# Performance work log

Hardware: AMD Instinct MI355X
Metric: run time of the kernel (lower is better)

## Reference

```python
import jax, jax.numpy as jnp
import numpy as np

B, C, D, H, EXP = 4, 1024, 1024, 16, 4
EPS = 1e-6


def ffn_layernorm(x, w, b):
    # normalize over channel axis (dim 1); w,b have shape (1, C)
    u = jnp.mean(x, axis=1, keepdims=True)
    s = jnp.mean((x - u) ** 2, axis=1, keepdims=True)
    xn = (x - u) / jnp.sqrt(s + EPS)
    return w[:, :, None] * xn + b[:, :, None]


def softmax_one(x):
    # exp(x - max) / (1 + sum exp(x - max)), exactly as the torch SoftmaxOne
    m = jnp.max(x, axis=-1, keepdims=True)
    e = jnp.exp(x - m)
    return e / (1.0 + jnp.sum(e, axis=-1, keepdims=True))


def setup_inputs() -> dict:
    key = jax.random.key(0)
    ks = jax.random.split(key, 20)
    n = lambda k, shape, s=0.02: jax.random.normal(k, shape, dtype=jnp.float32) * s
    inp = {
        "x1": jax.random.normal(ks[0], (B, C, D), dtype=jnp.float32),
        "lnq_w": jnp.ones((1, C), jnp.float32) + n(ks[1], (1, C)),
        "lnq_b": n(ks[2], (1, C)),
        "lnk_w": jnp.ones((1, C), jnp.float32) + n(ks[3], (1, C)),
        "lnk_b": n(ks[4], (1, C)),
        "lnv_w": jnp.ones((1, C), jnp.float32) + n(ks[5], (1, C)),
        "lnv_b": n(ks[6], (1, C)),
        "wq": n(ks[7], (D, D)),
        "bq": n(ks[8], (D,)),
        "wk": n(ks[9], (D, D)),
        "bk": n(ks[10], (D,)),
        "wv": n(ks[11], (D, D)),
        "bv": n(ks[12], (D,)),
        "ffnln_w": jnp.ones((1, C), jnp.float32) + n(ks[13], (1, C)),
        "ffnln_b": n(ks[14], (1, C)),
        "conv1_w": n(ks[15], (C * EXP, C)),
        "conv1_b": n(ks[16], (C * EXP,)),
        "conv2_w": n(ks[17], (C, C * EXP)),
        "conv2_b": n(ks[18], (C,)),
    }
    return inp


def reference(x1, lnq_w, lnq_b, lnk_w, lnk_b, lnv_w, lnv_b,
              wq, bq, wk, bk, wv, bv,
              ffnln_w, ffnln_b, conv1_w, conv1_b, conv2_w, conv2_b):
    b, c, d = x1.shape
    dh = d // H
    q = ffn_layernorm(x1, lnq_w, lnq_b)
    k = ffn_layernorm(x1, lnk_w, lnk_b)
    v = ffn_layernorm(x1, lnv_w, lnv_b)
    # nn.Linear: y = x @ W.T + b, then the torch code's direct reshape
    # (b, c, d) -> (b, H, c, dh) (NOT a transpose-split)
    q = (q @ wq.T + bq).reshape(b, H, c, dh)
    k = (k @ wk.T + bk).reshape(b, H, c, dh)
    v = (v @ wv.T + bv).reshape(b, H, c, dh)
    scale = 1.0 / np.sqrt(dh).astype(np.float32)
    attn = jnp.einsum("bhqe,bhke->bhqk", q * scale, k)
    attn_weights = softmax_one(attn)
    o = jnp.einsum("bhqk,bhke->bhqe", attn_weights, v)
    o = o.transpose(0, 2, 1, 3).reshape(b, c, d)
    x = x1 + o
    # FFN: channel LayerNorm -> 1x1 conv (channel mix) -> GELU -> 1x1 conv
    xl = ffn_layernorm(x, ffnln_w, ffnln_b)
    h1 = jnp.einsum("oc,bcl->bol", conv1_w, xl) + conv1_b[None, :, None]
    h1 = jax.nn.gelu(h1, approximate=False)
    h2 = jnp.einsum("oc,bcl->bol", conv2_w, h1) + conv2_b[None, :, None]
    return (x + h2, attn_weights)
```

## Files before the change

kernel.cpp:

```cpp
#include <hip/hip_runtime.h>
#include <hip/hip_bf16.h>
#include <math.h>


typedef __bf16 bf16;
typedef __bf16 bf16x4 __attribute__((ext_vector_type(4)));
typedef __bf16 bf16x8 __attribute__((ext_vector_type(8)));
typedef float floatx4 __attribute__((ext_vector_type(4)));

#define MFMA16(a, b, c) __builtin_amdgcn_mfma_f32_16x16x32_bf16(a, b, c, 0, 0, 0)

__device__ __forceinline__ void gload16(const void* g, void* l) {
    __builtin_amdgcn_global_load_lds((__attribute__((address_space(1))) void*)g,
                                     (__attribute__((address_space(3))) void*)l,
                                     16, 0, 0);
}

__global__ __launch_bounds__(256)
void cast_all(const float* __restrict__ s0, bf16* __restrict__ d0_,
              const float* __restrict__ s1, bf16* __restrict__ d1_,
              const float* __restrict__ s2, bf16* __restrict__ d2_,
              const float* __restrict__ s3, bf16* __restrict__ d3_,
              const float* __restrict__ s4, bf16* __restrict__ d4_,
              float* __restrict__ rsumout)
{
    __shared__ float S[64][4];
    const int blk = blockIdx.x;
    const int tid = threadIdx.x;
    if (blk >= 11264) {
        const int j = blk - 11264;
        const int seg = j >> 4;
        const int obase = (j & 15) << 6;
        const float* W = seg == 0 ? s0 : (seg == 1 ? s1 : s2);
        float* outr = rsumout + (seg << 10);
        const int lane = tid & 63, wv_ = tid >> 6;
        for (int oi = 0; oi < 64; ++oi) {
            const float4 w4 = *(const float4*)(W + ((long)(obase + oi) << 10) + (tid << 2));
            float p = w4.x + w4.y + w4.z + w4.w;
#pragma unroll
            for (int off = 1; off < 64; off <<= 1) p += __shfl_xor(p, off, 64);
            if (lane == 0) S[oi][wv_] = p;
        }
        __syncthreads();
        if (tid < 64)
            outr[obase + tid] = S[tid][0] + S[tid][1] + S[tid][2] + S[tid][3];
        return;
    }
    const float* s; bf16* d; int base;
    if (blk < 1024)      { s = s0; d = d0_; base = blk; }
    else if (blk < 2048) { s = s1; d = d1_; base = blk - 1024; }
    else if (blk < 3072) { s = s2; d = d2_; base = blk - 2048; }
    else if (blk < 7168) { s = s3; d = d3_; base = blk - 3072; }
    else                 { s = s4; d = d4_; base = blk - 7168; }
    long i = ((long)base << 10) + (tid << 2);
    float4 v = *(const float4*)(s + i);
    bf16x4 o;
    o[0] = (bf16)v.x; o[1] = (bf16)v.y; o[2] = (bf16)v.z; o[3] = (bf16)v.w;
    *(bf16x4*)(d + i) = o;
}

__global__ __launch_bounds__(256)
void stats_part(const float* __restrict__ xin, float* __restrict__ ps,
                float* __restrict__ pq)
{
    __shared__ float S1[4][64];
    __shared__ float S2[4][64];
    const int b = blockIdx.z, chunk = blockIdx.y;
    const int d0 = blockIdx.x << 6;
    const int tid = threadIdx.x;
    const int dl = tid & 63, cg = tid >> 6;
    const float* xp = xin + ((long)b << 20) + d0 + dl;
    const int cbase = (chunk << 8) + (cg << 6);
    float s = 0.f, sq = 0.f;
    for (int c = 0; c < 64; ++c) {
        float v = xp[(long)(cbase + c) << 10];
        s += v; sq += v * v;
    }
    S1[cg][dl] = s; S2[cg][dl] = sq;
    __syncthreads();
    if (tid < 64) {
        float ts = S1[0][tid] + S1[1][tid] + S1[2][tid] + S1[3][tid];
        float tq = S2[0][tid] + S2[1][tid] + S2[2][tid] + S2[3][tid];
        int idx = ((b * 4 + chunk) << 10) + d0 + tid;
        ps[idx] = ts; pq[idx] = tq;
    }
}

__global__ __launch_bounds__(256)
void ln_x1_kernel(const float* __restrict__ x1, const float* __restrict__ ps,
                  const float* __restrict__ pq, bf16* __restrict__ xn)
{
    const int bc = blockIdx.x;
    const int b = bc >> 10;
    const int d = threadIdx.x << 2;
    const long i = ((long)bc << 10) + d;
    const float* pb = ps + (b << 12) + d;
    const float* qb = pq + (b << 12) + d;
    float s0 = 0.f, s1 = 0.f, s2 = 0.f, s3 = 0.f;
    float q0 = 0.f, q1 = 0.f, q2 = 0.f, q3 = 0.f;
#pragma unroll
    for (int c4 = 0; c4 < 4; ++c4) {
        float4 pv = *(const float4*)(pb + (c4 << 10));
        float4 qv = *(const float4*)(qb + (c4 << 10));
        s0 += pv.x; s1 += pv.y; s2 += pv.z; s3 += pv.w;
        q0 += qv.x; q1 += qv.y; q2 += qv.z; q3 += qv.w;
    }
    const float inv1024 = 1.f / 1024.f;
    float u0 = s0 * inv1024, u1 = s1 * inv1024, u2 = s2 * inv1024, u3 = s3 * inv1024;
    float r0 = rsqrtf(q0 * inv1024 - u0 * u0 + 1e-6f);
    float r1 = rsqrtf(q1 * inv1024 - u1 * u1 + 1e-6f);
    float r2 = rsqrtf(q2 * inv1024 - u2 * u2 + 1e-6f);
    float r3 = rsqrtf(q3 * inv1024 - u3 * u3 + 1e-6f);
    const float4 xv = *(const float4*)(x1 + i);
    bf16x4 o;
    o[0] = (bf16)((xv.x - u0) * r0);
    o[1] = (bf16)((xv.y - u1) * r1);
    o[2] = (bf16)((xv.z - u2) * r2);
    o[3] = (bf16)((xv.w - u3) * r3);
    *(bf16x4*)(xn + i) = o;
}

template<int MODE>
__global__ __launch_bounds__(256, 3)
void gemm_nt(const bf16* __restrict__ Ab, const bf16* __restrict__ Bb,
             void* __restrict__ Outb, float* __restrict__ Part,
             const float* __restrict__ bias0, const float* __restrict__ bias1,
             const float* __restrict__ bias2, const float* __restrict__ residb,
             const float* __restrict__ lnw0, const float* __restrict__ lnw1,
             const float* __restrict__ lnw2,
             const float* __restrict__ lnbq, const float* __restrict__ lnbk,
             const float* __restrict__ lnbv, const float* __restrict__ rsum,
             long sAz, long sBz, long sOz, long sRz, long sPz,
             int M, int N, int K, int Ksub, int zdiv)
{
    __shared__ __align__(16) bf16 As[3][128 * 32];
    __shared__ __align__(16) bf16 Bs[3][128 * 32];
    const int z = blockIdx.z;
    const int zb = z / zdiv, kz = z % zdiv;
    const bf16* A = Ab + (long)zb * sAz + (long)kz * Ksub;
    const bf16* B = Bb + (long)zb * sBz + (long)kz * Ksub;
    const float* bias = (zb == 0) ? bias0 : (zb == 1 ? bias1 : bias2);
    const int m0 = blockIdx.y << 7, n0 = blockIdx.x << 7;
    const int tid = threadIdx.x;
    const int wave = tid >> 6, lane = tid & 63;
    const int wm = (wave & 1) << 6, wn = (wave >> 1) << 6;
    const int lm = lane & 15, quad = lane >> 4;
    const long rA0 = (long)(tid >> 2) * K;
    const long rA1 = (long)((tid >> 2) + 64) * K;
    const int kc8 = (tid & 3) << 3;
    const bf16* Ag = A + (long)m0 * K + kc8;
    const bf16* Bg = B + (long)n0 * K + kc8;
    const int nt = Ksub >> 5;
    floatx4 acc[4][4] = {};

    auto STAGE = [&](int pf_, int kt_) {
        gload16(Ag + rA0 + kt_, &As[pf_][tid << 3]);
        gload16(Ag + rA1 + kt_, &As[pf_][(tid + 256) << 3]);
        gload16(Bg + rA0 + kt_, &Bs[pf_][tid << 3]);
        gload16(Bg + rA1 + kt_, &Bs[pf_][(tid + 256) << 3]);
    };

    STAGE(0, 0);
    STAGE(1, 32);
    asm volatile("s_waitcnt vmcnt(4)" ::: "memory");
    __builtin_amdgcn_s_barrier();

    int cur = 0;
    for (int t = 0; t < nt; ++t) {
        if (t + 2 < nt) {
            int pf = cur - 1; if (pf < 0) pf += 3;
            STAGE(pf, (t + 2) << 5);
        }
        bf16x8 af[4], bfv[4];
#pragma unroll
        for (int i = 0; i < 4; ++i) {
            af[i]  = *(const bf16x8*)(&As[cur][((wm + i * 16 + lm) << 5) + (quad << 3)]);
            bfv[i] = *(const bf16x8*)(&Bs[cur][((wn + i * 16 + lm) << 5) + (quad << 3)]);
        }
        __builtin_amdgcn_s_setprio(1);
#pragma unroll
        for (int mi = 0; mi < 4; ++mi)
#pragma unroll
            for (int ni = 0; ni < 4; ++ni)
                acc[mi][ni] = MFMA16(af[mi], bfv[ni], acc[mi][ni]);
        __builtin_amdgcn_s_setprio(0);
        if (t + 2 < nt) asm volatile("s_waitcnt vmcnt(4)" ::: "memory");
        else            asm volatile("s_waitcnt vmcnt(0)" ::: "memory");
        __builtin_amdgcn_s_barrier();
        cur = (cur == 2) ? 0 : cur + 1;
    }

    const int quad4 = quad << 2;
    if (MODE == 2) {
        if (kz == 0) {
            float* Out = (float*)Outb + (long)zb * sOz;
            const float* R = residb + (long)zb * sRz;
#pragma unroll
            for (int mi = 0; mi < 4; ++mi)
#pragma unroll
                for (int ni = 0; ni < 4; ++ni)
#pragma unroll
                    for (int r = 0; r < 4; ++r) {
                        int row = m0 + wm + mi * 16 + quad4 + r;
                        int col = n0 + wn + ni * 16 + lm;
                        long idx = (long)row * N + col;
                        Out[idx] = acc[mi][ni][r] + bias[row] + R[idx];
                    }
        } else {
            float* Out = Part + (long)zb * sPz;
#pragma unroll
            for (int mi = 0; mi < 4; ++mi)
#pragma unroll
                for (int ni = 0; ni < 4; ++ni)
#pragma unroll
                    for (int r = 0; r < 4; ++r) {
                        int row = m0 + wm + mi * 16 + quad4 + r;
                        int col = n0 + wn + ni * 16 + lm;
                        Out[(long)row * N + col] = acc[mi][ni][r];
                    }
        }
    } else if (MODE == 0) {
        bf16* Out = (bf16*)Outb + (long)zb * sOz;
        const float* lw = (zb == 0) ? lnw0 : (zb == 1 ? lnw1 : lnw2);
        const float* lb = (zb == 0) ? lnbq : (zb == 1 ? lnbk : lnbv);
        const float* rs = rsum + (zb << 10);
#pragma unroll
        for (int mi = 0; mi < 4; ++mi)
#pragma unroll
            for (int r = 0; r < 4; ++r) {
                const int row = m0 + wm + mi * 16 + quad4 + r;
                const int crow = row & 1023;
                const float lwv = lw[crow], lbv = lb[crow];
#pragma unroll
                for (int ni = 0; ni < 4; ++ni) {
                    int col = n0 + wn + ni * 16 + lm;
                    float v = lwv * acc[mi][ni][r] + lbv * rs[col] + bias[col];
                    Out[(long)row * N + col] = (bf16)v;
                }
            }
    } else {
        bf16* Out = (bf16*)Outb + (long)zb * sOz;
#pragma unroll
        for (int mi = 0; mi < 4; ++mi)
#pragma unroll
            for (int ni = 0; ni < 4; ++ni)
#pragma unroll
                for (int r = 0; r < 4; ++r) {
                    int row = m0 + wm + mi * 16 + quad4 + r;
                    int col = n0 + wn + ni * 16 + lm;
                    float v = acc[mi][ni][r] + bias[col];
                    v = 0.5f * v * (1.0f + erff(v * 0.70710678118654752f));
                    Out[(long)row * N + col] = (bf16)v;
                }
    }
}

__global__ __launch_bounds__(256)
void addpart(float* __restrict__ out, const float* __restrict__ part)
{
    long i = (((long)blockIdx.x << 8) + threadIdx.x) << 2;
    float4 o = *(const float4*)(out + i);
    float4 p = *(const float4*)(part + i);
    o.x += p.x; o.y += p.y; o.z += p.z; o.w += p.w;
    *(float4*)(out + i) = o;
}

__global__ __launch_bounds__(256)
void vtrans_kernel(const bf16* __restrict__ v, bf16* __restrict__ vt)
{
    __shared__ bf16 T[64][66];
    const int p = blockIdx.y;
    const int k0 = blockIdx.x << 6;
    const bf16* V = v + ((long)p << 16);
    bf16* Vt = vt + ((long)p << 16);
    const int tid = threadIdx.x;
    const int e = tid & 63, g = tid >> 6;
#pragma unroll
    for (int j = 0; j < 16; ++j) {
        int kk = (g << 4) + j;
        T[e][kk] = V[((long)(k0 + kk) << 6) + e];
    }
    __syncthreads();
#pragma unroll
    for (int j = 0; j < 16; ++j) {
        int er = (g << 4) + j;
        Vt[((long)er << 10) + k0 + e] = T[er][e];
    }
}

__global__ __launch_bounds__(256)
void attn_kernel(const bf16* __restrict__ q, const bf16* __restrict__ k,
                 const bf16* __restrict__ vt, const float* __restrict__ x1,
                 float* __restrict__ attw, float* __restrict__ x)
{
    __shared__ __align__(16) bf16 Wl[16][1032];
    __shared__ float red[16][4];
    const int bid = blockIdx.x;
    const int p = ((bid & 7) << 3) | ((bid >> 3) & 7);
    const int s = bid >> 6;
    const int b = p >> 4, h = p & 15;
    const bf16* Qp = q + ((long)b << 20) + ((long)h << 16);
    const bf16* Kp = k + ((long)b << 20) + ((long)h << 16);
    const bf16* Vt = vt + ((long)p << 16);
    const int tid = threadIdx.x, w = tid >> 6, lane = tid & 63;
    const int lm = lane & 15, quad = lane >> 4;
    const int r0 = s << 4, kc0 = w << 8;

    floatx4 acc[16];
#pragma unroll
    for (int t = 0; t < 16; ++t) acc[t] = (floatx4){0.f, 0.f, 0.f, 0.f};

#pragma unroll
    for (int e0 = 0; e0 < 64; e0 += 32) {
        bf16x8 aq = *(const bf16x8*)(Qp + ((long)(r0 + lm) << 6) + e0 + quad * 8);
#pragma unroll
        for (int t = 0; t < 16; ++t) {
            bf16x8 bk = *(const bf16x8*)(Kp + ((long)(kc0 + t * 16 + lm) << 6) + e0 + quad * 8);
            acc[t] = MFMA16(aq, bk, acc[t]);
        }
    }
#pragma unroll
    for (int t = 0; t < 16; ++t)
#pragma unroll
        for (int r = 0; r < 4; ++r) acc[t][r] *= 0.125f;

    float mloc[4];
#pragma unroll
    for (int r = 0; r < 4; ++r) {
        float mm = acc[0][r];
#pragma unroll
        for (int t = 1; t < 16; ++t) mm = fmaxf(mm, acc[t][r]);
        mloc[r] = mm;
    }
#pragma unroll
    for (int off = 1; off < 16; off <<= 1)
#pragma unroll
        for (int r = 0; r < 4; ++r) mloc[r] = fmaxf(mloc[r], __shfl_xor(mloc[r], off, 64));
    if (lm == 0)
#pragma unroll
        for (int r = 0; r < 4; ++r) red[quad * 4 + r][w] = mloc[r];
    __syncthreads();
    float mfin[4];
#pragma unroll
    for (int r = 0; r < 4; ++r) {
        int row = quad * 4 + r;
        mfin[r] = fmaxf(fmaxf(red[row][0], red[row][1]), fmaxf(red[row][2], red[row][3]));
    }
    float sloc[4] = {0.f, 0.f, 0.f, 0.f};
#pragma unroll
    for (int t = 0; t < 16; ++t)
#pragma unroll
        for (int r = 0; r < 4; ++r) {
            float e = __expf(acc[t][r] - mfin[r]);
            acc[t][r] = e;
            sloc[r] += e;
        }
#pragma unroll
    for (int off = 1; off < 16; off <<= 1)
#pragma unroll
        for (int r = 0; r < 4; ++r) sloc[r] += __shfl_xor(sloc[r], off, 64);
    __syncthreads();
    if (lm == 0)
#pragma unroll
        for (int r = 0; r < 4; ++r) red[quad * 4 + r][w] = sloc[r];
    __syncthreads();
    float inv[4];
#pragma unroll
    for (int r = 0; r < 4; ++r) {
        int row = quad * 4 + r;
        inv[r] = 1.f / (1.f + red[row][0] + red[row][1] + red[row][2] + red[row][3]);
    }
#pragma unroll
    for (int r = 0; r < 4; ++r) {
        int row = quad * 4 + r;
        float iv = inv[r];
#pragma unroll
        for (int t = 0; t < 16; ++t)
            Wl[row][kc0 + t * 16 + lm] = (bf16)(acc[t][r] * iv);
    }
    __syncthreads();

    floatx4 opv[4];
#pragma unroll
    for (int ni = 0; ni < 4; ++ni) opv[ni] = (floatx4){0.f, 0.f, 0.f, 0.f};
#pragma unroll
    for (int i = 0; i < 8; ++i) {
        const int kk = kc0 + i * 32;
        bf16x8 a0 = *(const bf16x8*)&Wl[lm][kk + quad * 8];
#pragma unroll
        for (int ni = 0; ni < 4; ++ni) {
            bf16x8 bv = *(const bf16x8*)(Vt + ((long)(ni * 16 + lm) << 10) + kk + quad * 8);
            opv[ni] = MFMA16(a0, bv, opv[ni]);
        }
    }
    {
        float* attp = attw + ((long)p << 20) + ((long)r0 << 10);
#pragma unroll
        for (int i = 0; i < 16; ++i) {
            int v4 = (i << 8) + tid;
            int row = v4 >> 8, col = (v4 & 255) << 2;
            bf16x4 wv = *(const bf16x4*)&Wl[row][col];
            floatx4 o = {(float)wv[0], (float)wv[1], (float)wv[2], (float)wv[3]};
            __builtin_nontemporal_store(o, (floatx4*)(attp + ((long)row << 10) + col));
        }
    }
    __syncthreads();
    float* Ored = (float*)&Wl[0][0];
#pragma unroll
    for (int ni = 0; ni < 4; ++ni)
#pragma unroll
        for (int r = 0; r < 4; ++r)
            Ored[(w * 16 + quad * 4 + r) * 64 + ni * 16 + lm] = opv[ni][r];
    __syncthreads();
    const float* x1p = x1 + ((long)b << 20) + ((long)r0 << 10) + (h << 6);
    float* xp = x + ((long)b << 20) + ((long)r0 << 10) + (h << 6);
#pragma unroll
    for (int j = 0; j < 4; ++j) {
        int el = tid + (j << 8);
        int row = el >> 6, cc = el & 63;
        float o = Ored[row * 64 + cc] + Ored[(16 + row) * 64 + cc]
                + Ored[(32 + row) * 64 + cc] + Ored[(48 + row) * 64 + cc];
        xp[((long)row << 10) + cc] = x1p[((long)row << 10) + cc] + o;
    }
}

__global__ __launch_bounds__(256)
void ln_ffn_t_kernel(const float* __restrict__ x, const float* __restrict__ ps,
                     const float* __restrict__ pq, const float* __restrict__ fw,
                     const float* __restrict__ fb, bf16* __restrict__ xlT)
{
    __shared__ bf16 T[64][66];
    const int b = blockIdx.z;
    const int l0 = blockIdx.x << 6, c0 = blockIdx.y << 6;
    const int tid = threadIdx.x;
    const int ll = tid & 63, g = tid >> 6;
    float s = 0.f, q = 0.f;
#pragma unroll
    for (int c4 = 0; c4 < 4; ++c4) {
        s += ps[(b << 12) + (c4 << 10) + l0 + ll];
        q += pq[(b << 12) + (c4 << 10) + l0 + ll];
    }
    const float uu = s * (1.f / 1024.f);
    const float rr = rsqrtf(q * (1.f / 1024.f) - uu * uu + 1e-6f);
#pragma unroll
    for (int j = 0; j < 16; ++j) {
        int cc = (g << 4) + j;
        float v = x[((long)b << 20) + ((long)(c0 + cc) << 10) + l0 + ll];
        T[ll][cc] = (bf16)(fw[c0 + cc] * (v - uu) * rr + fb[c0 + cc]);
    }
    __syncthreads();
#pragma unroll
    for (int j = 0; j < 16; ++j) {
        int lr = (g << 4) + j;
        xlT[((long)b << 20) + ((long)(l0 + lr) << 10) + c0 + ll] = T[lr][ll];
    }
}

extern "C" void kernel_launch(void* const* d_in, const int* in_sizes, int n_in,
                              void* d_out, int out_size, void* d_ws, size_t ws_size,
                              hipStream_t stream)
{
    const float* x1      = (const float*)d_in[0];
    const float* lnq_w   = (const float*)d_in[1];
    const float* lnq_b   = (const float*)d_in[2];
    const float* lnk_w   = (const float*)d_in[3];
    const float* lnk_b   = (const float*)d_in[4];
    const float* lnv_w   = (const float*)d_in[5];
    const float* lnv_b   = (const float*)d_in[6];
    const float* wq      = (const float*)d_in[7];
    const float* bq      = (const float*)d_in[8];
    const float* wk      = (const float*)d_in[9];
    const float* bk      = (const float*)d_in[10];
    const float* wv      = (const float*)d_in[11];
    const float* bv      = (const float*)d_in[12];
    const float* ffnln_w = (const float*)d_in[13];
    const float* ffnln_b = (const float*)d_in[14];
    const float* conv1_w = (const float*)d_in[15];
    const float* conv1_b = (const float*)d_in[16];
    const float* conv2_w = (const float*)d_in[17];
    const float* conv2_b = (const float*)d_in[18];
    (void)in_sizes; (void)n_in; (void)out_size; (void)ws_size;

    char* ws = (char*)d_ws;
    const size_t OFF_VT   = 262144;
    const size_t OFF_QKV  = OFF_VT   + 8388608;
    const size_t OFF_WQKV = OFF_QKV  + 25165824;
    const size_t OFF_W1   = OFF_WQKV + 8388608;
    const size_t OFF_X    = OFF_W1   + 8388608;
    const size_t OFF_W2   = OFF_X    + 16777216;
    float* rsum  = (float*)(ws + 0);
    float* ps    = (float*)(ws + 65536);
    float* pq    = (float*)(ws + 131072);
    bf16*  vt    = (bf16*)(ws + OFF_VT);
    bf16*  qkv   = (bf16*)(ws + OFF_QKV);
    bf16*  wqkvb = (bf16*)(ws + OFF_WQKV);
    bf16*  w1b   = (bf16*)(ws + OFF_W1);
    float* x     = (float*)(ws + OFF_X);
    bf16*  w2b   = (bf16*)(ws + OFF_W2);
    bf16*  h1T   = (bf16*)(ws + OFF_VT);
    bf16*  xlT   = (bf16*)(ws + OFF_WQKV);
    float* part  = (float*)(ws + OFF_WQKV);

    float* out0 = (float*)d_out;
    float* attw = (float*)((char*)d_out + 16777216);
    bf16*  xn   = (bf16*)attw;

    cast_all<<<11312, 256, 0, stream>>>(wq, wqkvb, wk, wqkvb + (1 << 20),
                                        wv, wqkvb + (2 << 20), conv1_w, w1b, conv2_w, w2b,
                                        rsum);
    stats_part<<<dim3(16, 4, 4), 256, 0, stream>>>(x1, ps, pq);
    ln_x1_kernel<<<4096, 256, 0, stream>>>(x1, ps, pq, xn);
    gemm_nt<0><<<dim3(8, 32, 3), 256, 0, stream>>>(xn, wqkvb, qkv, nullptr,
                                                   bq, bk, bv, nullptr,
                                                   lnq_w, lnk_w, lnv_w,
                                                   lnq_b, lnk_b, lnv_b, rsum,
                                                   0, 1L << 20, 1L << 22, 0, 0,
                                                   4096, 1024, 1024, 1024, 1);
    vtrans_kernel<<<dim3(16, 64), 256, 0, stream>>>(qkv + (2L << 22), vt);
    attn_kernel<<<4096, 256, 0, stream>>>(qkv, qkv + (1L << 22), vt, x1, attw, x);
    stats_part<<<dim3(16, 4, 4), 256, 0, stream>>>(x, ps, pq);
    ln_ffn_t_kernel<<<dim3(16, 16, 4), 256, 0, stream>>>(x, ps, pq, ffnln_w, ffnln_b, xlT);
    gemm_nt<1><<<dim3(32, 8, 4), 256, 0, stream>>>(xlT, w1b, h1T, nullptr,
                                                   conv1_b, conv1_b, conv1_b, nullptr,
                                                   nullptr, nullptr, nullptr,
                                                   nullptr, nullptr, nullptr, nullptr,
                                                   1L << 20, 0, 1L << 22, 0, 0,
                                                   1024, 4096, 1024, 1024, 1);
    gemm_nt<2><<<dim3(8, 8, 8), 256, 0, stream>>>(w2b, h1T, out0, part,
                                                  conv2_b, conv2_b, conv2_b, x,
                                                  nullptr, nullptr, nullptr,
                                                  nullptr, nullptr, nullptr, nullptr,
                                                  0, 1L << 22, 1L << 20, 1L << 20,
                                                  1L << 20, 1024, 1024, 4096, 2048, 2);
    addpart<<<4096, 256, 0, stream>>>(out0, part);
}
```

Measured before the change: 657.9 us.

## Fuse stats into cast kernel, double-buffer GEMM, use tanh-form GELU

```diff
diff --git a/kernel.cpp b/kernel.cpp
--- a/kernel.cpp
+++ b/kernel.cpp
@@ -22,11 +22,38 @@
               const float* __restrict__ s2, bf16* __restrict__ d2_,
               const float* __restrict__ s3, bf16* __restrict__ d3_,
               const float* __restrict__ s4, bf16* __restrict__ d4_,
-              float* __restrict__ rsumout)
+              float* __restrict__ rsumout,
+              const float* __restrict__ x1, float* __restrict__ ps,
+              float* __restrict__ pq)
 {
     __shared__ float S[64][4];
+    __shared__ float S1[4][64];
+    __shared__ float S2[4][64];
     const int blk = blockIdx.x;
     const int tid = threadIdx.x;
+    if (blk >= 11312) {
+        const int j = blk - 11312;
+        const int d0 = (j & 15) << 6;
+        const int chunk = (j >> 4) & 3;
+        const int b = j >> 6;
+        const int dl = tid & 63, cg = tid >> 6;
+        const float* xp = x1 + ((long)b << 20) + d0 + dl;
+        const int cbase = (chunk << 8) + (cg << 6);
+        float s = 0.f, sq = 0.f;
+        for (int c = 0; c < 64; ++c) {
+            float v = xp[(long)(cbase + c) << 10];
+            s += v; sq += v * v;
+        }
+        S1[cg][dl] = s; S2[cg][dl] = sq;
+        __syncthreads();
+        if (tid < 64) {
+            float ts = S1[0][tid] + S1[1][tid] + S1[2][tid] + S1[3][tid];
+            float tq = S2[0][tid] + S2[1][tid] + S2[2][tid] + S2[3][tid];
+            int idx = ((b * 4 + chunk) << 10) + d0 + tid;
+            ps[idx] = ts; pq[idx] = tq;
+        }
+        return;
+    }
     if (blk >= 11264) {
         const int j = blk - 11264;
         const int seg = j >> 4;
@@ -133,8 +160,8 @@
              long sAz, long sBz, long sOz, long sRz, long sPz,
              int M, int N, int K, int Ksub, int zdiv)
 {
-    __shared__ __align__(16) bf16 As[3][128 * 32];
-    __shared__ __align__(16) bf16 Bs[3][128 * 32];
+    __shared__ __align__(16) bf16 As[2][128 * 32];
+    __shared__ __align__(16) bf16 Bs[2][128 * 32];
     const int z = blockIdx.z;
     const int zb = z / zdiv, kz = z % zdiv;
     const bf16* A = Ab + (long)zb * sAz + (long)kz * Ksub;
@@ -145,31 +172,33 @@
     const int wave = tid >> 6, lane = tid & 63;
     const int wm = (wave & 1) << 6, wn = (wave >> 1) << 6;
     const int lm = lane & 15, quad = lane >> 4;
-    const long rA0 = (long)(tid >> 2) * K;
-    const long rA1 = (long)((tid >> 2) + 64) * K;
-    const int kc8 = (tid & 3) << 3;
-    const bf16* Ag = A + (long)m0 * K + kc8;
-    const bf16* Bg = B + (long)n0 * K + kc8;
+    const bf16* Ag = A + (long)m0 * K;
+    const bf16* Bg = B + (long)n0 * K;
     const int nt = Ksub >> 5;
     floatx4 acc[4][4] = {};
 
-    auto STAGE = [&](int pf_, int kt_) {
-        gload16(Ag + rA0 + kt_, &As[pf_][tid << 3]);
-        gload16(Ag + rA1 + kt_, &As[pf_][(tid + 256) << 3]);
-        gload16(Bg + rA0 + kt_, &Bs[pf_][tid << 3]);
-        gload16(Bg + rA1 + kt_, &Bs[pf_][(tid + 256) << 3]);
-    };
-
-    STAGE(0, 0);
-    STAGE(1, 32);
-    asm volatile("s_waitcnt vmcnt(4)" ::: "memory");
-    __builtin_amdgcn_s_barrier();
-
-    int cur = 0;
+#pragma unroll
+    for (int r_ = 0; r_ < 2; ++r_) {
+        int s_ = (r_ << 8) + tid;
+        int lrow = s_ >> 2;
+        long go = (long)lrow * K + ((s_ & 3) << 3);
+        gload16(Ag + go, &As[0][s_ << 3]);
+        gload16(Bg + go, &Bs[0][s_ << 3]);
+    }
+    __syncthreads();
+
     for (int t = 0; t < nt; ++t) {
-        if (t + 2 < nt) {
-            int pf = cur - 1; if (pf < 0) pf += 3;
-            STAGE(pf, (t + 2) << 5);
+        const int cur = t & 1;
+        if (t + 1 < nt) {
+            const int kofs = (t + 1) << 5;
+#pragma unroll
+            for (int r_ = 0; r_ < 2; ++r_) {
+                int s_ = (r_ << 8) + tid;
+                int lrow = s_ >> 2;
+                long go = (long)lrow * K + kofs + ((s_ & 3) << 3);
+                gload16(Ag + go, &As[cur ^ 1][s_ << 3]);
+                gload16(Bg + go, &Bs[cur ^ 1][s_ << 3]);
+            }
         }
         bf16x8 af[4], bfv[4];
 #pragma unroll
@@ -184,10 +213,7 @@
             for (int ni = 0; ni < 4; ++ni)
                 acc[mi][ni] = MFMA16(af[mi], bfv[ni], acc[mi][ni]);
         __builtin_amdgcn_s_setprio(0);
-        if (t + 2 < nt) asm volatile("s_waitcnt vmcnt(4)" ::: "memory");
-        else            asm volatile("s_waitcnt vmcnt(0)" ::: "memory");
-        __builtin_amdgcn_s_barrier();
-        cur = (cur == 2) ? 0 : cur + 1;
+        __syncthreads();
     }
 
     const int quad4 = quad << 2;
@@ -249,7 +275,8 @@
                     int row = m0 + wm + mi * 16 + quad4 + r;
                     int col = n0 + wn + ni * 16 + lm;
                     float v = acc[mi][ni][r] + bias[col];
-                    v = 0.5f * v * (1.0f + erff(v * 0.70710678118654752f));
+                    float g = 1.5957691216f * v + 0.0713548162f * v * v * v;
+                    v = v / (1.0f + __expf(-g));
                     Out[(long)row * N + col] = (bf16)v;
                 }
     }
@@ -505,10 +532,9 @@
     float* attw = (float*)((char*)d_out + 16777216);
     bf16*  xn   = (bf16*)attw;
 
-    cast_all<<<11312, 256, 0, stream>>>(wq, wqkvb, wk, wqkvb + (1 << 20),
+    cast_all<<<11568, 256, 0, stream>>>(wq, wqkvb, wk, wqkvb + (1 << 20),
                                         wv, wqkvb + (2 << 20), conv1_w, w1b, conv2_w, w2b,
-                                        rsum);
-    stats_part<<<dim3(16, 4, 4), 256, 0, stream>>>(x1, ps, pq);
+                                        rsum, x1, ps, pq);
     ln_x1_kernel<<<4096, 256, 0, stream>>>(x1, ps, pq, xn);
     gemm_nt<0><<<dim3(8, 32, 3), 256, 0, stream>>>(xn, wqkvb, qkv, nullptr,
                                                    bq, bk, bv, nullptr,
```

Result: faster. 637.3 us (-3.1%).
